# Kernel optimization log

Measured on AMD Instinct MI355X. Metric: run time of the kernel, lower is better.

## Reference

```python
import jax, jax.numpy as jnp
import numpy as np
from jax import lax

B, LS, LT, C, H, GRID = 32, 256, 128, 768, 12, 16
KEEP_RATIO = 0.7

def _ln(x, w, b):
    mu = x.mean(-1, keepdims=True)
    var = ((x - mu) ** 2).mean(-1, keepdims=True)
    return (x - mu) / jnp.sqrt(var + 1e-5) * w + b

def _gelu(x):
    return jax.nn.gelu(x, approximate=False)

def setup_inputs() -> dict:
    key = jax.random.key(0)
    ks = jax.random.split(key, 16)
    w = lambda k, s: jax.random.normal(k, s, jnp.float32) * 0.02
    N = LT + LS
    return {
        'x': jax.random.normal(ks[0], (B, N, C), jnp.float32),
        'global_index_template': jax.random.randint(ks[1], (B, LT), 0, LT).astype(jnp.int32),
        'global_index_search': jax.random.randint(ks[2], (B, LS), 0, LS).astype(jnp.int32),
        'learn_template_mask': jax.random.uniform(ks[3], (2, B, LT // 2), jnp.float32),
        'ln1_w': jnp.ones((C,), jnp.float32), 'ln1_b': jnp.zeros((C,), jnp.float32),
        'qkv_w': w(ks[4], (C, 3 * C)),
        'proj_w': w(ks[5], (C, C)), 'proj_b': jnp.zeros((C,), jnp.float32),
        'ln2_w': jnp.ones((C,), jnp.float32), 'ln2_b': jnp.zeros((C,), jnp.float32),
        'fc1_w': w(ks[6], (C, 4 * C)), 'fc1_b': jnp.zeros((4 * C,), jnp.float32),
        'fc2_w': w(ks[7], (4 * C, C)), 'fc2_b': jnp.zeros((C,), jnp.float32),
        'd1_w': w(ks[8], (3 * C, 768)), 'd1_b': jnp.zeros((768,), jnp.float32),
        'd2_w': w(ks[9], (768, 384)), 'd2_b': jnp.zeros((384,), jnp.float32),
        'd3_w': w(ks[10], (384, 192)), 'd3_b': jnp.zeros((192,), jnp.float32),
        'd4_w': w(ks[11], (192, 1)), 'd4_b': jnp.zeros((1,), jnp.float32),
    }

def reference(x, global_index_template, global_index_search, learn_template_mask,
              ln1_w, ln1_b, qkv_w, proj_w, proj_b, ln2_w, ln2_b,
              fc1_w, fc1_b, fc2_w, fc2_b,
              d1_w, d1_b, d2_w, d2_b, d3_w, d3_b, d4_w, d4_b):
    bs = x.shape[0]
    lt = global_index_template.shape[1]
    ls = global_index_search.shape[1]
    half = lt // 2
    # --- roimax target representations ---
    init_rep = jnp.max(x[:, :half] * learn_template_mask[0][..., None], axis=1, keepdims=True)   # [B,1,C]
    dyn_rep = jnp.max(x[:, half:lt] * learn_template_mask[1][..., None], axis=1, keepdims=True)  # [B,1,C]
    feat = jnp.concatenate([x[:, -ls:],
                            jnp.broadcast_to(init_rep, (bs, ls, C)),
                            jnp.broadcast_to(dyn_rep, (bs, ls, C))], axis=-1)  # [B,ls,3C]
    h = _gelu(feat @ d1_w + d1_b)
    h = _gelu(h @ d2_w + d2_b)
    h = _gelu(h @ d3_w + d3_b)
    pred = h @ d4_w + d4_b                      # [B,ls,1]
    probs = jax.nn.sigmoid(pred)                # foreground probabilities
    # --- 3x3 region-sum conv and argmax center ---
    grid = probs.reshape(bs, 1, GRID, GRID)
    kern = jnp.ones((1, 1, 3, 3), grid.dtype)
    filt = lax.conv_general_dilated(grid, kern, (1, 1), 'SAME',
                                    dimension_numbers=('NCHW', 'OIHW', 'NCHW'))
    max_idx = jnp.argmax(filt.reshape(bs, -1), axis=1)
    cx, cy = max_idx // GRID, max_idx % GRID
    gx = jnp.arange(GRID)[None, :, None]
    gy = jnp.arange(GRID)[None, None, :]
    win = lambda r: ((jnp.abs(gx - cx[:, None, None]) <= r) &
                     (jnp.abs(gy - cy[:, None, None]) <= r)).reshape(bs, GRID * GRID)
    mask7, mask11 = win(3), win(5)
    foreground = (probs > 0.5).astype(jnp.int32)          # [B,ls,1]
    selected_fg = foreground * mask7[..., None].astype(jnp.int32)
    # --- candidate elimination: keep all tokens inside 11x11 window first, then top prob ---
    lens_keep = int(np.ceil(KEEP_RATIO * ls))
    p_out = jnp.where(mask11, jnp.inf, probs[..., 0])     # [B,ls]
    order = jnp.argsort(-p_out, axis=1)                   # stable descending
    topk_idx, non_topk = order[:, :lens_keep], order[:, lens_keep:]
    keep_index = jnp.take_along_axis(global_index_search, topk_idx, axis=1)
    removed_index = jnp.take_along_axis(global_index_search, non_topk, axis=1)
    xs = jnp.take_along_axis(x[:, lt:], topk_idx[..., None], axis=1)  # [B,lens_keep,C]
    xnew = jnp.concatenate([x[:, :lt], xs], axis=1)       # [B, lt+lens_keep, C]
    sf = jnp.take_along_axis(selected_fg, topk_idx[..., None], axis=1)[..., 0]
    decision = jax.nn.one_hot(sf, 2, dtype=x.dtype)       # scatter_(2, sf, 1)
    search_policy = jnp.concatenate([jnp.zeros((bs, lens_keep, 2), x.dtype), decision], -1)
    template_policy = jnp.zeros((bs, half, 4), x.dtype).at[:, :, 0].set(1.0)
    dynamic_policy = jnp.zeros((bs, half, 4), x.dtype).at[:, :, 1].set(1.0)
    P = jnp.concatenate([template_policy, dynamic_policy, search_policy], axis=1)
    key_bg = P[:, :, 2] > 0.5    # background search tokens -> masked as attention keys
    # --- attention ---
    n = xnew.shape[1]
    dh = C // H
    hn = _ln(xnew, ln1_w, ln1_b)
    qkv = (hn @ qkv_w).reshape(bs, n, 3, H, dh).transpose(2, 0, 3, 1, 4)
    q, k, v = qkv[0], qkv[1], qkv[2]
    scores = jnp.einsum('bhnd,bhmd->bhnm', q, k) * dh ** -0.5
    scores = jnp.where(key_bg[:, None, None, :], -1e9, scores)
    attn = jax.nn.softmax(scores, axis=-1)
    out = jnp.einsum('bhnm,bhmd->bhnd', attn, v).transpose(0, 2, 1, 3).reshape(bs, n, C)
    xnew = xnew + (out @ proj_w + proj_b)
    m = _ln(xnew, ln2_w, ln2_b)
    xout = xnew + (_gelu(m @ fc1_w + fc1_b) @ fc2_w + fc2_b)
    return (xout, keep_index, removed_index, attn)
```

## Files before the change

### kernel.cpp

```cpp
#include <hip/hip_runtime.h>
#include <hip/hip_bf16.h>
#include <math.h>

#define BB 32
#define LSN 256
#define LTN 128
#define CCH 768
#define NHH 12
#define NTOK 384
#define NKEEP 180
#define NREM 76
#define NNEW 308
#define MS 8192
#define MN 9856

typedef unsigned short u16;
typedef __attribute__((ext_vector_type(8))) short s8v;
typedef __attribute__((ext_vector_type(4))) float f4v;

__device__ __forceinline__ u16 f2bf(float x) {
    union { __hip_bfloat16 b; u16 u; } c; c.b = __float2bfloat16(x); return c.u;
}
__device__ __forceinline__ float bf2f(u16 u) {
    return __uint_as_float(((unsigned)u) << 16);
}
__device__ __forceinline__ void gl_lds16(const u16* g, u16* l) {
    __builtin_amdgcn_global_load_lds((const __attribute__((address_space(1))) unsigned*)g,
                                     (__attribute__((address_space(3))) unsigned*)l, 16, 0, 0);
}

__global__ void k_fail(float* o, float v) { o[0] = v; }

__global__ void k_reps(const float* __restrict__ x, const float* __restrict__ mask,
                       float* __restrict__ rep0, float* __restrict__ rep1) {
    int b = blockIdx.x, t = threadIdx.x;
    for (int c = t; c < CCH; c += 256) {
        float m0 = -INFINITY, m1 = -INFINITY;
        for (int i = 0; i < 64; ++i) {
            float v0 = x[(size_t)(b * NTOK + i) * CCH + c] * mask[b * 64 + i];
            float v1 = x[(size_t)(b * NTOK + 64 + i) * CCH + c] * mask[BB * 64 + b * 64 + i];
            m0 = fmaxf(m0, v0); m1 = fmaxf(m1, v1);
        }
        rep0[b * CCH + c] = m0; rep1[b * CCH + c] = m1;
    }
}

__device__ __forceinline__ float gelu_np(float v) {
    float t = v / 1.4142135623730951f;
    float ef = (float)erf((double)t);
    return 0.5f * v * (1.0f + ef);
}

template<int ROWMAP>
__global__ __launch_bounds__(256) void gemm_exact(const float* __restrict__ A,
                                                  const float* __restrict__ rep0, const float* __restrict__ rep1,
                                                  const float* __restrict__ W, const float* __restrict__ bias,
                                                  float* __restrict__ out, int N, int K) {
    __shared__ float As[32 * 64];
    __shared__ float Bs[32 * 64];
    int t = threadIdx.x;
    int tx = t & 15, ty = t >> 4;
    int bm = blockIdx.y * 64, bn = blockIdx.x * 64;
    int b = bm >> 8;
    float acc[4][4] = {};

    int arow = t >> 2;
    int ak = (t & 3) * 4;
    int asw = arow ^ ((ak & 4) << 2);
    size_t aoff;
    if (ROWMAP) aoff = (size_t)(b * NTOK + LTN + ((bm + arow) & 255)) * CCH;
    else        aoff = (size_t)(bm + arow) * K;

    int bkr = t >> 4, bc = (t & 15) * 4;

#define LOADA(kg) (ROWMAP ? (((kg) < CCH) ? *(const float4*)&A[aoff + (kg)] \
                    : (((kg) < 2*CCH) ? *(const float4*)&rep0[b*CCH + (kg) - CCH] \
                                      : *(const float4*)&rep1[b*CCH + (kg) - 2*CCH])) \
                   : *(const float4*)&A[aoff + (kg)])

    int nt = K >> 5;
    float4 ra0 = LOADA(ak), ra1 = LOADA(16 + ak);
    float4 rb0 = *(const float4*)&W[(size_t)bkr * N + bn + bc];
    float4 rb1 = *(const float4*)&W[(size_t)(16 + bkr) * N + bn + bc];

    for (int tile = 0; tile < nt; ++tile) {
        __syncthreads();
        As[(ak + 0) * 64 + asw] = ra0.x; As[(ak + 1) * 64 + asw] = ra0.y;
        As[(ak + 2) * 64 + asw] = ra0.z; As[(ak + 3) * 64 + asw] = ra0.w;
        As[(16 + ak + 0) * 64 + asw] = ra1.x; As[(16 + ak + 1) * 64 + asw] = ra1.y;
        As[(16 + ak + 2) * 64 + asw] = ra1.z; As[(16 + ak + 3) * 64 + asw] = ra1.w;
        *(float4*)&Bs[t * 4] = rb0;
        *(float4*)&Bs[1024 + t * 4] = rb1;
        if (tile + 1 < nt) {
            int k0 = (tile + 1) << 5;
            ra0 = LOADA(k0 + ak); ra1 = LOADA(k0 + 16 + ak);
            rb0 = *(const float4*)&W[(size_t)(k0 + bkr) * N + bn + bc];
            rb1 = *(const float4*)&W[(size_t)(k0 + 16 + bkr) * N + bn + bc];
        }
        __syncthreads();
#pragma unroll
        for (int k = 0; k < 32; ++k) {
            float a[4], bv[4];
            *(float4*)&a[0]  = *(const float4*)&As[k * 64 + ((ty * 4) ^ ((k & 4) << 2))];
            *(float4*)&bv[0] = *(const float4*)&Bs[k * 64 + tx * 4];
#pragma unroll
            for (int i = 0; i < 4; ++i)
#pragma unroll
                for (int j = 0; j < 4; ++j) acc[i][j] = fmaf(a[i], bv[j], acc[i][j]);
        }
    }
#undef LOADA
#pragma unroll
    for (int i = 0; i < 4; ++i) {
        int m = bm + ty * 4 + i;
        float4 o;
        o.x = gelu_np(acc[i][0] + bias[bn + tx * 4 + 0]);
        o.y = gelu_np(acc[i][1] + bias[bn + tx * 4 + 1]);
        o.z = gelu_np(acc[i][2] + bias[bn + tx * 4 + 2]);
        o.w = gelu_np(acc[i][3] + bias[bn + tx * 4 + 3]);
        *(float4*)&out[(size_t)m * N + bn + tx * 4] = o;
    }
}

__global__ void k_d4(const float* __restrict__ h3, const float* __restrict__ w4,
                     const float* __restrict__ b4, float* __restrict__ probs) {
    int m = blockIdx.x * 256 + threadIdx.x;
    if (m >= MS) return;
    float acc = 0.f;
    for (int k = 0; k < 192; ++k) acc = fmaf(h3[(size_t)m * 192 + k], w4[k], acc);
    float pred = acc + b4[0];
    float ef = (float)exp(-(double)pred);
    probs[m] = 1.0f / (1.0f + ef);
}

__global__ void k_select(const float* __restrict__ probs, float* __restrict__ pout, int* __restrict__ sf) {
    int b = blockIdx.x, t = threadIdx.x;
    __shared__ float pr[256];
    __shared__ double ft[256];
    __shared__ int cxy[2];
    pr[t] = probs[b * 256 + t];
    __syncthreads();
    int X = t >> 4, Y = t & 15;
    double s = 0.0;
    for (int dx = -1; dx <= 1; ++dx)
        for (int dy = -1; dy <= 1; ++dy) {
            int xx = X + dx, yy = Y + dy;
            if (xx >= 0 && xx < 16 && yy >= 0 && yy < 16) s += (double)pr[xx * 16 + yy];
        }
    ft[t] = s;
    __syncthreads();
    if (t == 0) {
        double best = ft[0]; int bi = 0;
        for (int i = 1; i < 256; ++i) if (ft[i] > best) { best = ft[i]; bi = i; }
        cxy[0] = bi >> 4; cxy[1] = bi & 15;
    }
    __syncthreads();
    int cx = cxy[0], cy = cxy[1];
    int ax = X - cx; if (ax < 0) ax = -ax;
    int ay = Y - cy; if (ay < 0) ay = -ay;
    bool m7  = (ax <= 3) && (ay <= 3);
    bool m11 = (ax <= 5) && (ay <= 5);
    int fg = (pr[t] > 0.5f) ? 1 : 0;
    sf[b * 256 + t] = m7 ? fg : 0;
    pout[b * 256 + t] = m11 ? INFINITY : pr[t];
}

__global__ void k_sort(const float* __restrict__ pout, const int* __restrict__ sf, const int* __restrict__ gis,
                       float* __restrict__ keep_out, float* __restrict__ rem_out,
                       int* __restrict__ topk, int* __restrict__ keybg) {
    int b = blockIdx.x, t = threadIdx.x;
    __shared__ float p[256];
    __shared__ int ord[256];
    p[t] = pout[b * 256 + t];
    __syncthreads();
    float pi = p[t];
    int rank = 0;
    for (int j = 0; j < 256; ++j) {
        float pj = p[j];
        rank += (pj > pi) || (pj == pi && j < t);
    }
    ord[rank] = t;
    __syncthreads();
    int idx = ord[t];
    int g = gis[b * 256 + idx];
    if (t < NKEEP) {
        keep_out[b * NKEEP + t] = (float)g;
        topk[b * NKEEP + t] = idx;
        keybg[b * NNEW + LTN + t] = (sf[b * 256 + idx] == 0) ? 1 : 0;
    } else {
        rem_out[b * NREM + (t - NKEEP)] = (float)g;
    }
    if (t < LTN) keybg[b * NNEW + t] = 0;
}

__global__ void k_xnew(const float* __restrict__ x, const int* __restrict__ topk, float* __restrict__ xn) {
    int row = blockIdx.x;
    int b = row / NNEW, r = row - b * NNEW;
    int src = (r < LTN) ? r : (LTN + topk[b * NKEEP + (r - LTN)]);
    const float* s = x + (size_t)(b * NTOK + src) * CCH;
    float* d = xn + (size_t)row * CCH;
    for (int c = threadIdx.x; c < CCH; c += 256) d[c] = s[c];
}


__global__ void k_ln_bf(const float* __restrict__ in, const float* __restrict__ w, const float* __restrict__ b,
                        u16* __restrict__ out) {
    int row = blockIdx.x, t = threadIdx.x;
    __shared__ float s1[256], s2[256];
    const float* p = in + (size_t)row * CCH;
    float v[3]; float a0 = 0.f, a1 = 0.f;
#pragma unroll
    for (int i = 0; i < 3; ++i) { v[i] = p[t + 256 * i]; a0 += v[i]; a1 += v[i] * v[i]; }
    s1[t] = a0; s2[t] = a1;
    __syncthreads();
    for (int off = 128; off > 0; off >>= 1) {
        if (t < off) { s1[t] += s1[t + off]; s2[t] += s2[t + off]; }
        __syncthreads();
    }
    float mu = s1[0] * (1.0f / CCH);
    float var = s2[0] * (1.0f / CCH) - mu * mu;
    float rstd = rsqrtf(var + 1e-5f);
#pragma unroll
    for (int i = 0; i < 3; ++i) {
        int c = t + 256 * i;
        out[(size_t)row * CCH + c] = f2bf((v[i] - mu) * rstd * w[c] + b[c]);
    }
}

__global__ void k_wT(const float* __restrict__ W, u16* __restrict__ Wt, int K, int N) {
    __shared__ float tile[32][33];
    int k0 = blockIdx.x * 32, n0 = blockIdx.y * 32;
    int tx = threadIdx.x, ty = threadIdx.y;
    for (int i = ty; i < 32; i += 8) tile[i][tx] = W[(size_t)(k0 + i) * N + n0 + tx];
    __syncthreads();
    for (int i = ty; i < 32; i += 8) Wt[(size_t)(n0 + i) * K + k0 + tx] = f2bf(tile[tx][i]);
}

template<int MODE>
__global__ __launch_bounds__(256) void gemm_bf16(const u16* __restrict__ A, const u16* __restrict__ Bt,
                                                 const float* __restrict__ bias, const float* __restrict__ res,
                                                 float* __restrict__ outf, u16* __restrict__ outb,
                                                 u16* __restrict__ vT, int N, int K) {
    __shared__ u16 sm[2][2][4096];
    int t = threadIdx.x, lane = t & 63, wid = t >> 6;
    int bm = blockIdx.y * 128, bn = blockIdx.x * 128;
    const u16* pA[2]; const u16* pB[2];
#pragma unroll
    for (int i = 0; i < 2; ++i) {
        int L = wid * 128 + i * 64 + lane;
        int line = L >> 3, sp = L & 7, sl = sp ^ (line & 7);
        int r = (line << 1) | (sl >> 2), k0 = (sl & 3) << 3;
        pA[i] = A + (size_t)(bm + r) * K + k0;
        pB[i] = Bt + (size_t)(bn + r) * K + k0;
    }
    int wr = wid >> 1, wc = wid & 1;
    int l15 = lane & 15, l4 = lane >> 4;
    int rA = wr * 64 + l15, rB = wc * 64 + l15;
    int offA = (rA >> 1) * 128 + (((((rA & 1) << 2) | l4)) ^ ((rA >> 1) & 7)) * 16;
    int offB = (rB >> 1) * 128 + (((((rB & 1) << 2) | l4)) ^ ((rB >> 1) & 7)) * 16;
    f4v zero = {0.f, 0.f, 0.f, 0.f};
    f4v acc[4][4];
#pragma unroll
    for (int i = 0; i < 4; ++i)
#pragma unroll
        for (int j = 0; j < 4; ++j) acc[i][j] = zero;

#define STAGE_G(buf, kt) { \
    u16* da = &sm[buf][0][wid * 1024]; u16* db = &sm[buf][1][wid * 1024]; \
    gl_lds16(pA[0] + (kt) * 32, da); \
    gl_lds16(pA[1] + (kt) * 32, da + 512); \
    gl_lds16(pB[0] + (kt) * 32, db); \
    gl_lds16(pB[1] + (kt) * 32, db + 512); \
}
    int nk = K >> 5;
    STAGE_G(0, 0);
    __syncthreads();
    for (int kt = 0; kt < nk; ++kt) {
        int cur = kt & 1;
        if (kt + 1 < nk) STAGE_G(cur ^ 1, kt + 1);
        const char* bA = (const char*)&sm[cur][0][0];
        const char* bBp = (const char*)&sm[cur][1][0];
        s8v a[4], b[4];
#pragma unroll
        for (int i = 0; i < 4; ++i) {
            a[i] = *(const s8v*)(bA + offA + i * 1024);
            b[i] = *(const s8v*)(bBp + offB + i * 1024);
        }
#pragma unroll
        for (int mf = 0; mf < 4; ++mf)
#pragma unroll
            for (int nf = 0; nf < 4; ++nf)
                acc[mf][nf] = __builtin_amdgcn_mfma_f32_16x16x32_bf16(a[mf], b[nf], acc[mf][nf], 0, 0, 0);
        __syncthreads();
    }
#undef STAGE_G
#pragma unroll
    for (int mf = 0; mf < 4; ++mf)
#pragma unroll
        for (int nf = 0; nf < 4; ++nf)
#pragma unroll
            for (int j = 0; j < 4; ++j) {
                int row = bm + wr * 64 + mf * 16 + l4 * 4 + j;
                int col = bn + wc * 64 + nf * 16 + l15;
                float v = acc[mf][nf][j];
                if (MODE == 0) {
                    if (col < 1536) {
                        if (col < 768) v *= 0.125f;
                        outb[(size_t)row * 1536 + col] = f2bf(v);
                    } else {
                        int c2 = col - 1536, hh = c2 >> 6, dd = c2 & 63;
                        int bb = row / NNEW, tok = row - bb * NNEW;
                        vT[(((size_t)bb * NHH + hh) * 64 + dd) * 312 + tok] = f2bf(v);
                    }
                } else if (MODE == 1) {
                    outf[(size_t)row * N + col] = v + bias[col] + res[(size_t)row * N + col];
                } else {
                    float g = v + bias[col];
                    g = 0.5f * g * (1.0f + erff(g * 0.70710678f));
                    outb[(size_t)row * N + col] = f2bf(g);
                }
            }
}

__global__ __launch_bounds__(256) void k_attn2(const u16* __restrict__ qkvQK, const u16* __restrict__ vT,
                                               const int* __restrict__ keybg,
                                               float* __restrict__ attn_out, u16* __restrict__ ctx) {
    __shared__ __align__(16) char smem[98560];
    u16* Qs = (u16*)smem;
    u16* Ks = (u16*)(smem + 9216);
    u16* Ss = (u16*)(smem + 55296);
    int* kb = (int*)(smem + 97280);
    float* OT = (float*)Ss;
    u16* Vts = Ks;

    int bh = blockIdx.y; int b = bh / NHH, h = bh % NHH;
    int q0 = blockIdx.x * 64;
    int nq = NNEW - q0; if (nq > 64) nq = 64;
    int t = threadIdx.x, lane = t & 63, wid = t >> 6;
    int l15 = lane & 15, l4 = lane >> 4;
    s8v z = {0, 0, 0, 0, 0, 0, 0, 0};

    {
        int r = t >> 2, c = (t & 3) * 16;
        u16* dst = Qs + r * 72 + c;
        if (r < nq) {
            const u16* src = qkvQK + (size_t)(b * NNEW + q0 + r) * 1536 + h * 64 + c;
            *(s8v*)dst = *(const s8v*)src;
            *(s8v*)(dst + 8) = *(const s8v*)(src + 8);
        } else { *(s8v*)dst = z; *(s8v*)(dst + 8) = z; }
    }
    for (int it = 0; it < 5; ++it) {
        int r = it * 64 + (t >> 2), c = (t & 3) * 16;
        u16* dst = Ks + r * 72 + c;
        if (r < NNEW) {
            const u16* src = qkvQK + (size_t)(b * NNEW + r) * 1536 + 768 + h * 64 + c;
            *(s8v*)dst = *(const s8v*)src;
            *(s8v*)(dst + 8) = *(const s8v*)(src + 8);
        } else { *(s8v*)dst = z; *(s8v*)(dst + 8) = z; }
    }
    for (int i = t; i < 320; i += 256) kb[i] = (i < NNEW) ? keybg[b * NNEW + i] : 1;
    __syncthreads();

    f4v zero = {0.f, 0.f, 0.f, 0.f};
    f4v acc[4][5];
#pragma unroll
    for (int i = 0; i < 4; ++i)
#pragma unroll
        for (int j = 0; j < 5; ++j) acc[i][j] = zero;
#pragma unroll
    for (int ks = 0; ks < 2; ++ks) {
        s8v a[4], bf[5];
#pragma unroll
        for (int mf = 0; mf < 4; ++mf) a[mf] = *(const s8v*)(Qs + (mf * 16 + l15) * 72 + ks * 32 + l4 * 8);
#pragma unroll
        for (int nf = 0; nf < 5; ++nf) bf[nf] = *(const s8v*)(Ks + (wid * 80 + nf * 16 + l15) * 72 + ks * 32 + l4 * 8);
#pragma unroll
        for (int mf = 0; mf < 4; ++mf)
#pragma unroll
            for (int nf = 0; nf < 5; ++nf)
                acc[mf][nf] = __builtin_amdgcn_mfma_f32_16x16x32_bf16(a[mf], bf[nf], acc[mf][nf], 0, 0, 0);
    }
#pragma unroll
    for (int nf = 0; nf < 5; ++nf) {
        int n = wid * 80 + nf * 16 + l15;
        int msk = kb[n];
#pragma unroll
        for (int mf = 0; mf < 4; ++mf)
#pragma unroll
            for (int j = 0; j < 4; ++j) {
                int q = mf * 16 + l4 * 4 + j;
                float v = msk ? -1e9f : acc[mf][nf][j];
                Ss[q * 328 + n] = f2bf(v);
            }
    }
    __syncthreads();

    {
        int d = t >> 2;
        for (int c = (t & 3); c < 39; c += 4) {
            const u16* src = vT + ((size_t)bh * 64 + d) * 312 + c * 8;
            *(s8v*)(Vts + d * 312 + c * 8) = *(const s8v*)src;
        }
    }
    {
        int q = t >> 2, j4 = t & 3;
        u16* row = Ss + q * 328 + j4 * 80;
        float mx = -3e38f;
#pragma unroll
        for (int i = 0; i < 10; ++i) {
            s8v vv = *(const s8v*)(row + i * 8);
#pragma unroll
            for (int e = 0; e < 8; ++e) mx = fmaxf(mx, bf2f((u16)vv[e]));
        }
        mx = fmaxf(mx, __shfl_xor(mx, 1));
        mx = fmaxf(mx, __shfl_xor(mx, 2));
        float sum = 0.f;
#pragma unroll
        for (int i = 0; i < 10; ++i) {
            s8v vv = *(const s8v*)(row + i * 8);
            s8v ov;
#pragma unroll
            for (int e = 0; e < 8; ++e) {
                float ex = expf(bf2f((u16)vv[e]) - mx);
                sum += ex;
                ov[e] = (short)f2bf(ex);
            }
            *(s8v*)(row + i * 8) = ov;
        }
        sum += __shfl_xor(sum, 1);
        sum += __shfl_xor(sum, 2);
        float inv = 1.0f / sum;
#pragma unroll
        for (int i = 0; i < 10; ++i) {
            s8v vv = *(const s8v*)(row + i * 8);
            s8v ov;
            float pf[8];
#pragma unroll
            for (int e = 0; e < 8; ++e) {
                float p = bf2f((u16)vv[e]) * inv;
                pf[e] = p;
                ov[e] = (short)f2bf(p);
            }
            *(s8v*)(row + i * 8) = ov;
            if (q < nq) {
                int n0 = j4 * 80 + i * 8;
                float* dst = attn_out + ((size_t)bh * NNEW + q0 + q) * NNEW + n0;
#pragma unroll
                for (int e = 0; e < 8; ++e) if (n0 + e < NNEW) dst[e] = pf[e];
            }
        }
    }
    __syncthreads();

    f4v o[4];
#pragma unroll
    for (int i = 0; i < 4; ++i) o[i] = zero;
    int dblk = wid * 16;
#pragma unroll
    for (int ks = 0; ks < 10; ++ks) {
        s8v av = *(const s8v*)(Vts + (dblk + l15) * 312 + ks * 32 + l4 * 8);
#pragma unroll
        for (int nf = 0; nf < 4; ++nf) {
            s8v pv = *(const s8v*)(Ss + (nf * 16 + l15) * 328 + ks * 32 + l4 * 8);
            o[nf] = __builtin_amdgcn_mfma_f32_16x16x32_bf16(av, pv, o[nf], 0, 0, 0);
        }
    }
    __syncthreads();
#pragma unroll
    for (int nf = 0; nf < 4; ++nf)
#pragma unroll
        for (int j = 0; j < 4; ++j)
            OT[(dblk + l4 * 4 + j) * 65 + nf * 16 + l15] = o[nf][j];
    __syncthreads();
    {
        int q = t >> 2, c = t & 3;
        if (q < nq) {
            u16 buf[16];
#pragma unroll
            for (int i = 0; i < 16; ++i) buf[i] = f2bf(OT[(c * 16 + i) * 65 + q]);
            u16* dst = ctx + (size_t)(b * NNEW + q0 + q) * CCH + h * 64 + c * 16;
            *(s8v*)dst = *(const s8v*)&buf[0];
            *(s8v*)(dst + 8) = *(const s8v*)&buf[8];
        }
    }
}

extern "C" void kernel_launch(void* const* d_in, const int* in_sizes, int n_in,
                              void* d_out, int out_size, void* d_ws, size_t ws_size,
                              hipStream_t stream) {
    const float* x     = (const float*)d_in[0];
    const int*   gis   = (const int*)d_in[2];
    const float* mask  = (const float*)d_in[3];
    const float* ln1w  = (const float*)d_in[4];
    const float* ln1b  = (const float*)d_in[5];
    const float* qkvw  = (const float*)d_in[6];
    const float* projw = (const float*)d_in[7];
    const float* projb = (const float*)d_in[8];
    const float* ln2w  = (const float*)d_in[9];
    const float* ln2b  = (const float*)d_in[10];
    const float* fc1w  = (const float*)d_in[11];
    const float* fc1b  = (const float*)d_in[12];
    const float* fc2w  = (const float*)d_in[13];
    const float* fc2b  = (const float*)d_in[14];
    const float* d1w   = (const float*)d_in[15];
    const float* d1b   = (const float*)d_in[16];
    const float* d2w   = (const float*)d_in[17];
    const float* d2b   = (const float*)d_in[18];
    const float* d3w   = (const float*)d_in[19];
    const float* d3b   = (const float*)d_in[20];
    const float* d4w   = (const float*)d_in[21];
    const float* d4b   = (const float*)d_in[22];

    float* out_x    = (float*)d_out;
    float* out_keep = out_x + 7569408;
    float* out_rem  = out_keep + 5760;
    float* out_attn = out_rem + 2432;

    char* ws = (char*)d_ws;
    u16* hn_bf  = (u16*)(ws);
    u16* qkvQK  = (u16*)(ws + 15138816);
    u16* vTb    = (u16*)(ws + 45416448);
    u16* fc1_bf = (u16*)(ws);
    u16* ctx_bf = (u16*)(ws + 60751872);
    u16* qkvwT  = (u16*)(ws + 75890688);
    u16* projwT = (u16*)(ws + 79429632);
    u16* fc1wT  = (u16*)(ws + 80609280);
    u16* fc2wT  = (u16*)(ws + 85327872);
    char* misc  = ws + 90046464;
    float* rep0  = (float*)(misc + 0 * 262144);
    float* rep1  = (float*)(misc + 1 * 262144);
    float* probs = (float*)(misc + 2 * 262144);
    float* pout  = (float*)(misc + 3 * 262144);
    int*   sf    = (int*)(misc + 4 * 262144);
    int*   topk  = (int*)(misc + 5 * 262144);
    int*   keybg = (int*)(misc + 6 * 262144);
    size_t required = 90046464ull + 7ull * 262144ull;
    if (ws_size < required) {
        k_fail<<<1, 1, 0, stream>>>((float*)d_out, (float)(ws_size / 1048576.0));
        return;
    }

    float* h1 = (float*)out_attn;
    float* h2 = h1 + 8192 * 768;
    float* h3 = h2 + 8192 * 384;

    k_wT<<<dim3(24, 72), dim3(32, 8), 0, stream>>>(qkvw, qkvwT, 768, 2304);
    k_wT<<<dim3(24, 24), dim3(32, 8), 0, stream>>>(projw, projwT, 768, 768);
    k_wT<<<dim3(24, 96), dim3(32, 8), 0, stream>>>(fc1w, fc1wT, 768, 3072);
    k_wT<<<dim3(96, 24), dim3(32, 8), 0, stream>>>(fc2w, fc2wT, 3072, 768);
    hipMemsetAsync(vTb, 0, 15335424, stream);

    k_reps<<<BB, 256, 0, stream>>>(x, mask, rep0, rep1);
    gemm_exact<1><<<dim3(12, 128), 256, 0, stream>>>(x, rep0, rep1, d1w, d1b, h1, 768, 2304);
    gemm_exact<0><<<dim3(6, 128), 256, 0, stream>>>(h1, nullptr, nullptr, d2w, d2b, h2, 384, 768);
    gemm_exact<0><<<dim3(3, 128), 256, 0, stream>>>(h2, nullptr, nullptr, d3w, d3b, h3, 192, 384);
    k_d4<<<MS / 256, 256, 0, stream>>>(h3, d4w, d4b, probs);
    k_select<<<BB, 256, 0, stream>>>(probs, pout, sf);
    k_sort<<<BB, 256, 0, stream>>>(pout, sf, gis, out_keep, out_rem, topk, keybg);
    k_xnew<<<MN, 256, 0, stream>>>(x, topk, out_x);

    k_ln_bf<<<MN, 256, 0, stream>>>(out_x, ln1w, ln1b, hn_bf);
    gemm_bf16<0><<<dim3(18, 77), 256, 0, stream>>>(hn_bf, qkvwT, nullptr, nullptr, nullptr, qkvQK, vTb, 2304, 768);
    k_attn2<<<dim3(5, 384), 256, 0, stream>>>(qkvQK, vTb, keybg, out_attn, ctx_bf);
    gemm_bf16<1><<<dim3(6, 77), 256, 0, stream>>>(ctx_bf, projwT, projb, out_x, out_x, nullptr, nullptr, 768, 768);
    k_ln_bf<<<MN, 256, 0, stream>>>(out_x, ln2w, ln2b, ctx_bf);
    gemm_bf16<2><<<dim3(24, 77), 256, 0, stream>>>(ctx_bf, fc1wT, fc1b, nullptr, nullptr, fc1_bf, nullptr, 3072, 768);
    gemm_bf16<1><<<dim3(6, 77), 256, 0, stream>>>(fc1_bf, fc2wT, fc2b, out_x, out_x, nullptr, nullptr, 768, 3072);
}
```

Measured before the change: 1.090 ms.

## Fuse prep, select/sort, gather+LN kernels and add XCD-aware block swizzle

Merges the four weight-transpose launches and the vTb memset into a single prep kernel. Fuses select with sort, and the row gather with LayerNorm1, which removes intermediate global round trips and several launches. Adds an XCD-aware remapping of block indices in the bf16 GEMM and attention kernels so neighbouring tiles land on the same XCD and share its L2. The swizzle reorders work but does not change what is computed.

New measurement: 1.039 ms. -4.7%, faster.

```diff
diff --git a/kernel.cpp b/kernel.cpp
--- a/kernel.cpp
+++ b/kernel.cpp
@@ -27,6 +27,11 @@
 __device__ __forceinline__ void gl_lds16(const u16* g, u16* l) {
     __builtin_amdgcn_global_load_lds((const __attribute__((address_space(1))) unsigned*)g,
                                      (__attribute__((address_space(3))) unsigned*)l, 16, 0, 0);
+}
+__device__ __forceinline__ int xcd_swz(int lin, int nwg) {
+    int q = nwg >> 3, r = nwg & 7;
+    int xcd = lin & 7, idx = lin >> 3;
+    return (xcd < r ? xcd * (q + 1) : r * (q + 1) + (xcd - r) * q) + idx;
 }
 
 __global__ void k_fail(float* o, float v) { o[0] = v; }
@@ -133,11 +138,16 @@
     probs[m] = 1.0f / (1.0f + ef);
 }
 
-__global__ void k_select(const float* __restrict__ probs, float* __restrict__ pout, int* __restrict__ sf) {
+__global__ void k_selsort(const float* __restrict__ probs, const int* __restrict__ gis,
+                          float* __restrict__ keep_out, float* __restrict__ rem_out,
+                          int* __restrict__ topk, int* __restrict__ keybg) {
     int b = blockIdx.x, t = threadIdx.x;
     __shared__ float pr[256];
     __shared__ double ft[256];
     __shared__ int cxy[2];
+    __shared__ float pout[256];
+    __shared__ int sf[256];
+    __shared__ int ord[256];
     pr[t] = probs[b * 256 + t];
     __syncthreads();
     int X = t >> 4, Y = t & 15;
@@ -161,22 +171,13 @@
     bool m7  = (ax <= 3) && (ay <= 3);
     bool m11 = (ax <= 5) && (ay <= 5);
     int fg = (pr[t] > 0.5f) ? 1 : 0;
-    sf[b * 256 + t] = m7 ? fg : 0;
-    pout[b * 256 + t] = m11 ? INFINITY : pr[t];
-}
-
-__global__ void k_sort(const float* __restrict__ pout, const int* __restrict__ sf, const int* __restrict__ gis,
-                       float* __restrict__ keep_out, float* __restrict__ rem_out,
-                       int* __restrict__ topk, int* __restrict__ keybg) {
-    int b = blockIdx.x, t = threadIdx.x;
-    __shared__ float p[256];
-    __shared__ int ord[256];
-    p[t] = pout[b * 256 + t];
-    __syncthreads();
-    float pi = p[t];
+    sf[t] = m7 ? fg : 0;
+    pout[t] = m11 ? INFINITY : pr[t];
+    __syncthreads();
+    float pi = pout[t];
     int rank = 0;
     for (int j = 0; j < 256; ++j) {
-        float pj = p[j];
+        float pj = pout[j];
         rank += (pj > pi) || (pj == pi && j < t);
     }
     ord[rank] = t;
@@ -186,20 +187,40 @@
     if (t < NKEEP) {
         keep_out[b * NKEEP + t] = (float)g;
         topk[b * NKEEP + t] = idx;
-        keybg[b * NNEW + LTN + t] = (sf[b * 256 + idx] == 0) ? 1 : 0;
+        keybg[b * NNEW + LTN + t] = (sf[idx] == 0) ? 1 : 0;
     } else {
         rem_out[b * NREM + (t - NKEEP)] = (float)g;
     }
     if (t < LTN) keybg[b * NNEW + t] = 0;
 }
 
-__global__ void k_xnew(const float* __restrict__ x, const int* __restrict__ topk, float* __restrict__ xn) {
-    int row = blockIdx.x;
-    int b = row / NNEW, r = row - b * NNEW;
-    int src = (r < LTN) ? r : (LTN + topk[b * NKEEP + (r - LTN)]);
-    const float* s = x + (size_t)(b * NTOK + src) * CCH;
-    float* d = xn + (size_t)row * CCH;
-    for (int c = threadIdx.x; c < CCH; c += 256) d[c] = s[c];
+__global__ void k_xnew_ln(const float* __restrict__ x, const int* __restrict__ topk,
+                          const float* __restrict__ w, const float* __restrict__ b,
+                          float* __restrict__ out_x, u16* __restrict__ hn) {
+    int row = blockIdx.x, t = threadIdx.x;
+    int bb = row / NNEW, r = row - bb * NNEW;
+    int src = (r < LTN) ? r : (LTN + topk[bb * NKEEP + (r - LTN)]);
+    const float* p = x + (size_t)(bb * NTOK + src) * CCH;
+    __shared__ float s1[256], s2[256];
+    float v[3]; float a0 = 0.f, a1 = 0.f;
+#pragma unroll
+    for (int i = 0; i < 3; ++i) { v[i] = p[t + 256 * i]; a0 += v[i]; a1 += v[i] * v[i]; }
+#pragma unroll
+    for (int i = 0; i < 3; ++i) out_x[(size_t)row * CCH + t + 256 * i] = v[i];
+    s1[t] = a0; s2[t] = a1;
+    __syncthreads();
+    for (int off = 128; off > 0; off >>= 1) {
+        if (t < off) { s1[t] += s1[t + off]; s2[t] += s2[t + off]; }
+        __syncthreads();
+    }
+    float mu = s1[0] * (1.0f / CCH);
+    float var = s2[0] * (1.0f / CCH) - mu * mu;
+    float rstd = rsqrtf(var + 1e-5f);
+#pragma unroll
+    for (int i = 0; i < 3; ++i) {
+        int c = t + 256 * i;
+        hn[(size_t)row * CCH + c] = f2bf((v[i] - mu) * rstd * w[c] + b[c]);
+    }
 }
 
 
@@ -227,13 +248,31 @@
     }
 }
 
-__global__ void k_wT(const float* __restrict__ W, u16* __restrict__ Wt, int K, int N) {
-    __shared__ float tile[32][33];
-    int k0 = blockIdx.x * 32, n0 = blockIdx.y * 32;
-    int tx = threadIdx.x, ty = threadIdx.y;
-    for (int i = ty; i < 32; i += 8) tile[i][tx] = W[(size_t)(k0 + i) * N + n0 + tx];
-    __syncthreads();
-    for (int i = ty; i < 32; i += 8) Wt[(size_t)(n0 + i) * K + k0 + tx] = f2bf(tile[tx][i]);
+__global__ void k_prep(const float* __restrict__ qkvw, const float* __restrict__ projw,
+                       const float* __restrict__ fc1w, const float* __restrict__ fc2w,
+                       u16* __restrict__ qkvwT, u16* __restrict__ projwT,
+                       u16* __restrict__ fc1wT, u16* __restrict__ fc2wT,
+                       u16* __restrict__ vTb) {
+    int id = blockIdx.x;
+    int t = threadIdx.x;
+    if (id >= 6912) {
+        size_t off = ((size_t)(id - 6912) * 256 + t) * 8;
+        s8v z = {0,0,0,0,0,0,0,0};
+        *(s8v*)(vTb + off) = z;
+        return;
+    }
+    const float* W; u16* Wt; int K, N, tile;
+    if (id < 1728)      { W = qkvw;  Wt = qkvwT;  K = 768;  N = 2304; tile = id; }
+    else if (id < 2304) { W = projw; Wt = projwT; K = 768;  N = 768;  tile = id - 1728; }
+    else if (id < 4608) { W = fc1w;  Wt = fc1wT;  K = 768;  N = 3072; tile = id - 2304; }
+    else                { W = fc2w;  Wt = fc2wT;  K = 3072; N = 768;  tile = id - 4608; }
+    int kt = K >> 5;
+    int k0 = (tile % kt) * 32, n0 = (tile / kt) * 32;
+    __shared__ float tilebuf[32][33];
+    int tx = t & 31, ty = t >> 5;
+    for (int i = ty; i < 32; i += 8) tilebuf[i][tx] = W[(size_t)(k0 + i) * N + n0 + tx];
+    __syncthreads();
+    for (int i = ty; i < 32; i += 8) Wt[(size_t)(n0 + i) * K + k0 + tx] = f2bf(tilebuf[tx][i]);
 }
 
 template<int MODE>
@@ -243,7 +282,11 @@
                                                  u16* __restrict__ vT, int N, int K) {
     __shared__ u16 sm[2][2][4096];
     int t = threadIdx.x, lane = t & 63, wid = t >> 6;
-    int bm = blockIdx.y * 128, bn = blockIdx.x * 128;
+    int nwg = gridDim.x * gridDim.y;
+    int lin = blockIdx.y * gridDim.x + blockIdx.x;
+    int T = xcd_swz(lin, nwg);
+    int bx = T % gridDim.x, by = T / gridDim.x;
+    int bm = by * 128, bn = bx * 128;
     const u16* pA[2]; const u16* pB[2];
 #pragma unroll
     for (int i = 0; i < 2; ++i) {
@@ -333,8 +376,12 @@
     float* OT = (float*)Ss;
     u16* Vts = Ks;
 
-    int bh = blockIdx.y; int b = bh / NHH, h = bh % NHH;
-    int q0 = blockIdx.x * 64;
+    int nwg = gridDim.x * gridDim.y;
+    int lin = blockIdx.y * gridDim.x + blockIdx.x;
+    int T = xcd_swz(lin, nwg);
+    int bh = T / 5;
+    int q0 = (T - bh * 5) * 64;
+    int b = bh / NHH, h = bh % NHH;
     int nq = NNEW - q0; if (nq > 64) nq = 64;
     int t = threadIdx.x, lane = t & 63, wid = t >> 6;
     int l15 = lane & 15, l4 = lane >> 4;
@@ -530,8 +577,6 @@
     float* rep0  = (float*)(misc + 0 * 262144);
     float* rep1  = (float*)(misc + 1 * 262144);
     float* probs = (float*)(misc + 2 * 262144);
-    float* pout  = (float*)(misc + 3 * 262144);
-    int*   sf    = (int*)(misc + 4 * 262144);
     int*   topk  = (int*)(misc + 5 * 262144);
     int*   keybg = (int*)(misc + 6 * 262144);
     size_t required = 90046464ull + 7ull * 262144ull;
@@ -544,22 +589,16 @@
     float* h2 = h1 + 8192 * 768;
     float* h3 = h2 + 8192 * 384;
 
-    k_wT<<<dim3(24, 72), dim3(32, 8), 0, stream>>>(qkvw, qkvwT, 768, 2304);
-    k_wT<<<dim3(24, 24), dim3(32, 8), 0, stream>>>(projw, projwT, 768, 768);
-    k_wT<<<dim3(24, 96), dim3(32, 8), 0, stream>>>(fc1w, fc1wT, 768, 3072);
-    k_wT<<<dim3(96, 24), dim3(32, 8), 0, stream>>>(fc2w, fc2wT, 3072, 768);
-    hipMemsetAsync(vTb, 0, 15335424, stream);
+    k_prep<<<10656, 256, 0, stream>>>(qkvw, projw, fc1w, fc2w, qkvwT, projwT, fc1wT, fc2wT, vTb);
 
     k_reps<<<BB, 256, 0, stream>>>(x, mask, rep0, rep1);
     gemm_exact<1><<<dim3(12, 128), 256, 0, stream>>>(x, rep0, rep1, d1w, d1b, h1, 768, 2304);
     gemm_exact<0><<<dim3(6, 128), 256, 0, stream>>>(h1, nullptr, nullptr, d2w, d2b, h2, 384, 768);
     gemm_exact<0><<<dim3(3, 128), 256, 0, stream>>>(h2, nullptr, nullptr, d3w, d3b, h3, 192, 384);
     k_d4<<<MS / 256, 256, 0, stream>>>(h3, d4w, d4b, probs);
-    k_select<<<BB, 256, 0, stream>>>(probs, pout, sf);
-    k_sort<<<BB, 256, 0, stream>>>(pout, sf, gis, out_keep, out_rem, topk, keybg);
-    k_xnew<<<MN, 256, 0, stream>>>(x, topk, out_x);
-
-    k_ln_bf<<<MN, 256, 0, stream>>>(out_x, ln1w, ln1b, hn_bf);
+    k_selsort<<<BB, 256, 0, stream>>>(probs, gis, out_keep, out_rem, topk, keybg);
+    k_xnew_ln<<<MN, 256, 0, stream>>>(x, topk, ln1w, ln1b, out_x, hn_bf);
+
     gemm_bf16<0><<<dim3(18, 77), 256, 0, stream>>>(hn_bf, qkvwT, nullptr, nullptr, nullptr, qkvQK, vTb, 2304, 768);
     k_attn2<<<dim3(5, 384), 256, 0, stream>>>(qkvQK, vTb, keybg, out_attn, ctx_bf);
     gemm_bf16<1><<<dim3(6, 77), 256, 0, stream>>>(ctx_bf, projwT, projb, out_x, out_x, nullptr, nullptr, 768, 768);
```
